# Kernel tuning notes

Hardware: AMD Instinct MI355X
Metric: run time of the kernel (lower is better)

Reference implementation:

```python
import jax, jax.numpy as jnp
import numpy as np

N = 50000        # num_nodes
D = 512          # input_dim == output_dim (residual update requires equality)
EU = 100000      # undirected edges; directed E = 2*EU = 200000
STEP = 0.5       # step_size


def setup_inputs() -> dict:
    key = jax.random.key(0)
    ks = jax.random.split(key, 5)
    x = jax.random.normal(ks[0], (N, D), jnp.float32)
    # symmetric edge list without self loops: store (s,d) then (d,s)
    src = jax.random.randint(ks[1], (EU,), 0, N, dtype=jnp.int32)
    off = jax.random.randint(ks[2], (EU,), 1, N, dtype=jnp.int32)
    dst = (src + off) % N
    edge_index = jnp.stack([jnp.concatenate([src, dst]),
                            jnp.concatenate([dst, src])])  # [2, 2*EU]
    # reverse-edge index: edge e < EU reverses to e+EU and vice versa
    ar = jnp.arange(EU, dtype=jnp.int32)
    right_idx = jnp.concatenate([ar + EU, ar])
    # params: nn.Linear(D, D) and sheaf_learner nn.Linear(2D, 1, bias=False)
    W_lin = jax.random.normal(ks[3], (D, D), jnp.float32) / np.sqrt(D)
    b_lin = jnp.zeros((D,), jnp.float32)
    w_sheaf = jax.random.normal(ks[4], (2 * D,), jnp.float32) / np.sqrt(2 * D)
    return {"x": x, "W_lin": W_lin, "b_lin": b_lin, "w_sheaf": w_sheaf,
            "edge_index": edge_index, "right_idx": right_idx}


def reference(x, W_lin, b_lin, w_sheaf, edge_index, right_idx):
    row, col = edge_index[0], edge_index[1]
    d = x.shape[1]
    # sheaf_learner(cat([x_row, x_col])) == (x @ w[:d])[row] + (x @ w[d:])[col]
    s = x @ w_sheaf[:d]                      # [N]
    t = x @ w_sheaf[d:]                      # [N]
    maps = jnp.tanh(s[row] + t[col])         # [E] scalar restriction maps
    # off-diagonal Laplacian values: -F_e(row) * F_reverse(e)
    non_diag = -maps * maps[right_idx]       # [E]
    diag_maps = jax.ops.segment_sum(maps ** 2, row, num_segments=N)  # [N]
    d_inv = (diag_maps + 1.0) ** -0.5        # [N]
    norm_maps = d_inv[row] * non_diag * d_inv[col]                   # [E]
    diag = d_inv * diag_maps * d_inv                                 # [N]
    # y = linear(x); L @ y done as diag term + edge scatter
    y = x @ W_lin.T + b_lin                  # [N, D]
    Ly = diag[:, None] * y + jax.ops.segment_sum(
        norm_maps[:, None] * y[col], row, num_segments=N)
    return x - STEP * Ly
```

## Files before the change

kernel.cpp:

```cpp
#include <hip/hip_runtime.h>
#include <hip/hip_bf16.h>
#include <cstdint>
#include <cstddef>


#define DD 512
#define STEPSZ 0.5f
#define SLOTS 32

typedef __bf16 bf16;
typedef __bf16 bf16x8 __attribute__((ext_vector_type(8)));
typedef __bf16 bf16x4 __attribute__((ext_vector_type(4)));
typedef float f32x4 __attribute__((ext_vector_type(4)));

#define GLOAD16(g, l)                                                     \
  __builtin_amdgcn_global_load_lds(                                       \
      (const __attribute__((address_space(1))) void*)(g),                 \
      (__attribute__((address_space(3))) void*)(l), 16, 0, 0)

__global__ __launch_bounds__(256) void k_convert_w(
    const float* __restrict__ w, bf16* __restrict__ wbf, int n) {
  int i = (blockIdx.x * 256 + threadIdx.x) * 4;
  if (i >= n) return;
  float4 v = *(const float4*)(w + i);
  bf16x4 p;
  p[0] = (bf16)v.x; p[1] = (bf16)v.y; p[2] = (bf16)v.z; p[3] = (bf16)v.w;
  *(bf16x4*)(wbf + i) = p;
}

__global__ __launch_bounds__(256) void k_convert_st(
    const float* __restrict__ x, const float* __restrict__ wsheaf,
    bf16* __restrict__ xbf, float* __restrict__ s, float* __restrict__ t,
    int n) {
  int lane = threadIdx.x & 63;
  int row = (blockIdx.x << 2) + (threadIdx.x >> 6);
  if (row >= n) return;
  const float* xr = x + (size_t)row * DD + lane * 8;
  float4 a = *(const float4*)xr;
  float4 b = *(const float4*)(xr + 4);
  bf16x8 p;
  p[0] = (bf16)a.x; p[1] = (bf16)a.y; p[2] = (bf16)a.z; p[3] = (bf16)a.w;
  p[4] = (bf16)b.x; p[5] = (bf16)b.y; p[6] = (bf16)b.z; p[7] = (bf16)b.w;
  *(bf16x8*)(xbf + (size_t)row * DD + lane * 8) = p;
  const float* w1 = wsheaf + lane * 8;
  const float* w2 = wsheaf + DD + lane * 8;
  float4 wa = *(const float4*)w1, wb = *(const float4*)(w1 + 4);
  float4 wc = *(const float4*)w2, wd = *(const float4*)(w2 + 4);
  float sv = a.x * wa.x + a.y * wa.y + a.z * wa.z + a.w * wa.w +
             b.x * wb.x + b.y * wb.y + b.z * wb.z + b.w * wb.w;
  float tv = a.x * wc.x + a.y * wc.y + a.z * wc.z + a.w * wc.w +
             b.x * wd.x + b.y * wd.y + b.z * wd.z + b.w * wd.w;
  #pragma unroll
  for (int o = 32; o > 0; o >>= 1) {
    sv += __shfl_xor(sv, o);
    tv += __shfl_xor(tv, o);
  }
  if (lane == 0) { s[row] = sv; t[row] = tv; }
}

__global__ __launch_bounds__(256) void k_fill(
    const int* __restrict__ ei, const float* __restrict__ s,
    const float* __restrict__ t, float* __restrict__ dmaps,
    int* __restrict__ fill, int* __restrict__ ccol, float* __restrict__ cval,
    int E) {
  int e = blockIdx.x * 256 + threadIdx.x;
  if (e >= E) return;
  int r = ei[e], c = ei[E + e];
  float sr = s[r], tc = t[c], sc = s[c], tr = t[r];
  float me = tanhf(sr + tc);
  float mr = tanhf(sc + tr);
  atomicAdd(dmaps + r, me * me);
  int p = atomicAdd(fill + r, 1);
  if (p < SLOTS) {
    ccol[(size_t)r * SLOTS + p] = c;
    cval[(size_t)r * SLOTS + p] = -me * mr;
  }
}

__global__ __launch_bounds__(256) void k_gemm(
    const bf16* __restrict__ xbf, const bf16* __restrict__ wbf,
    const float* __restrict__ bias, bf16* __restrict__ y, int M, int nwg) {
  __shared__ bf16 lds[16384];
  int orig = blockIdx.x;
  int q = nwg >> 3, r = nwg & 7;
  int xcd = orig & 7;
  int wgid = (xcd < r ? xcd * (q + 1) : r * (q + 1) + (xcd - r) * q) +
             (orig >> 3);
  int bm = wgid >> 2, bn = wgid & 3;
  int tid = threadIdx.x, w = tid >> 6, lane = tid & 63;
  int wr = w >> 1, wc = w & 1;
  int l7 = lane & 7, lhi = lane >> 4;

  int srow = lane >> 3;
  int kc = l7 ^ srow;
  const bf16* gA[4];
  const bf16* gB[4];
  bf16* lA[4];
  bf16* lB[4];
  #pragma unroll
  for (int j = 0; j < 4; ++j) {
    int rloc = w * 32 + j * 8 + srow;
    int ga = bm * 128 + rloc;
    if (ga > M - 1) ga = M - 1;
    gA[j] = xbf + (size_t)ga * DD + kc * 8;
    gB[j] = wbf + (size_t)(bn * 128 + rloc) * DD + kc * 8;
    lA[j] = lds + (w * 32 + j * 8) * 64;
    lB[j] = lds + 8192 + (w * 32 + j * 8) * 64;
  }

  f32x4 acc[4][4] = {};
  int arow = (wr * 64 + (lane & 15)) * 64;
  int brow = (wc * 64 + (lane & 15)) * 64;

  for (int k0 = 0; k0 < DD; k0 += 64) {
    #pragma unroll
    for (int j = 0; j < 4; ++j) {
      GLOAD16(gA[j] + k0, lA[j]);
      GLOAD16(gB[j] + k0, lB[j]);
    }
    __syncthreads();
    #pragma unroll
    for (int kw = 0; kw < 2; ++kw) {
      int sl = ((kw * 4 + lhi) ^ l7) * 8;
      bf16x8 af[4], bfr[4];
      #pragma unroll
      for (int m = 0; m < 4; ++m)
        af[m] = *(const bf16x8*)(lds + arow + m * 16 * 64 + sl);
      #pragma unroll
      for (int nn = 0; nn < 4; ++nn)
        bfr[nn] = *(const bf16x8*)(lds + 8192 + brow + nn * 16 * 64 + sl);
      #pragma unroll
      for (int m = 0; m < 4; ++m)
        #pragma unroll
        for (int nn = 0; nn < 4; ++nn)
          acc[m][nn] = __builtin_amdgcn_mfma_f32_16x16x32_bf16(
              af[m], bfr[nn], acc[m][nn], 0, 0, 0);
    }
    __syncthreads();
  }

  float bv[4];
  #pragma unroll
  for (int nn = 0; nn < 4; ++nn)
    bv[nn] = bias[bn * 128 + wc * 64 + nn * 16 + (lane & 15)];
  bf16* reg = lds + w * 4096;
  #pragma unroll
  for (int m = 0; m < 4; ++m)
    #pragma unroll
    for (int nn = 0; nn < 4; ++nn)
      #pragma unroll
      for (int rr = 0; rr < 4; ++rr) {
        int row = m * 16 + lhi * 4 + rr;
        int col = nn * 16 + (lane & 15);
        reg[row * 64 + (((col >> 3) ^ (row & 7)) << 3) + (col & 7)] =
            (bf16)(acc[m][nn][rr] + bv[nn]);
      }
  #pragma unroll
  for (int p = 0; p < 8; ++p) {
    int row = p * 8 + (lane >> 3);
    int slot = l7 ^ (row & 7);
    bf16x8 v = *(const bf16x8*)(reg + row * 64 + slot * 8);
    int grow = bm * 128 + wr * 64 + row;
    if (grow < M)
      *(bf16x8*)(y + (size_t)grow * DD + bn * 128 + wc * 64 + l7 * 8) = v;
  }
}

__global__ __launch_bounds__(256) void k_final(
    const float* __restrict__ x, const bf16* __restrict__ xb,
    const bf16* __restrict__ y, const float* __restrict__ dmaps,
    const int* __restrict__ fill, const int* __restrict__ ccol,
    const float* __restrict__ cval, float* __restrict__ out, int n,
    int use_bf) {
  int lane = threadIdx.x & 63;
  int row = (blockIdx.x << 2) + (threadIdx.x >> 6);
  if (row >= n) return;
  int c0 = lane * 8;
  bf16x8 yv = *(const bf16x8*)(y + (size_t)row * DD + c0);
  float dm = dmaps[row];
  float inv_r = rsqrtf(dm + 1.0f);
  float dg = dm / (dm + 1.0f);
  float acc[8];
  #pragma unroll
  for (int j = 0; j < 8; ++j) acc[j] = dg * (float)yv[j];
  int cnt = fill[row];
  if (cnt > SLOTS) cnt = SLOTS;
  const int* cc = ccol + (size_t)row * SLOTS;
  const float* cv = cval + (size_t)row * SLOTS;
  unsigned nm1 = (unsigned)(n - 1);
  for (int i = 0; i < cnt; i += 4) {
    int4 c4 = *(const int4*)(cc + i);
    float4 v4 = *(const float4*)(cv + i);
    int rem = cnt - i;
    unsigned ca = min((unsigned)c4.x, nm1);
    unsigned cb = min((unsigned)c4.y, nm1);
    unsigned cg = min((unsigned)c4.z, nm1);
    unsigned cd = min((unsigned)c4.w, nm1);
    bf16x8 na = *(const bf16x8*)(y + (size_t)ca * DD + c0);
    bf16x8 nb = *(const bf16x8*)(y + (size_t)cb * DD + c0);
    bf16x8 ng = *(const bf16x8*)(y + (size_t)cg * DD + c0);
    bf16x8 nd = *(const bf16x8*)(y + (size_t)cd * DD + c0);
    float va = rem > 0 ? v4.x * inv_r * rsqrtf(dmaps[ca] + 1.0f) : 0.0f;
    float vb = rem > 1 ? v4.y * inv_r * rsqrtf(dmaps[cb] + 1.0f) : 0.0f;
    float vg = rem > 2 ? v4.z * inv_r * rsqrtf(dmaps[cg] + 1.0f) : 0.0f;
    float vd = rem > 3 ? v4.w * inv_r * rsqrtf(dmaps[cd] + 1.0f) : 0.0f;
    #pragma unroll
    for (int j = 0; j < 8; ++j)
      acc[j] += va * (float)na[j] + vb * (float)nb[j] + vg * (float)ng[j] +
                vd * (float)nd[j];
  }
  float xr[8];
  if (use_bf) {
    bf16x8 xv = *(const bf16x8*)(xb + (size_t)row * DD + c0);
    #pragma unroll
    for (int j = 0; j < 8; ++j) xr[j] = (float)xv[j];
  } else {
    const float* xp = x + (size_t)row * DD + c0;
    float4 xa = *(const float4*)xp, xbv = *(const float4*)(xp + 4);
    xr[0] = xa.x; xr[1] = xa.y; xr[2] = xa.z; xr[3] = xa.w;
    xr[4] = xbv.x; xr[5] = xbv.y; xr[6] = xbv.z; xr[7] = xbv.w;
  }
  float4 o1, o2;
  o1.x = xr[0] - STEPSZ * acc[0]; o1.y = xr[1] - STEPSZ * acc[1];
  o1.z = xr[2] - STEPSZ * acc[2]; o1.w = xr[3] - STEPSZ * acc[3];
  o2.x = xr[4] - STEPSZ * acc[4]; o2.y = xr[5] - STEPSZ * acc[5];
  o2.z = xr[6] - STEPSZ * acc[6]; o2.w = xr[7] - STEPSZ * acc[7];
  float* outr = out + (size_t)row * DD + c0;
  *(float4*)outr = o1;
  *(float4*)(outr + 4) = o2;
}

extern "C" void kernel_launch(void* const* d_in, const int* in_sizes, int n_in,
                              void* d_out, int out_size, void* d_ws,
                              size_t ws_size, hipStream_t stream) {
  const float* x = (const float*)d_in[0];
  const float* W = (const float*)d_in[1];
  const float* b = (const float*)d_in[2];
  const float* wsheaf = (const float*)d_in[3];
  const int* ei = (const int*)d_in[4];
  const int* right = (const int*)d_in[5];
  (void)right;
  int N = in_sizes[0] / DD;
  int E = in_sizes[5];

  char* ws = (char*)d_ws;
  size_t p = 0;
  auto alloc = [&](size_t bytes) -> char* {
    char* r = ws + p;
    p += (bytes + 255) & ~(size_t)255;
    return r;
  };
  bf16* yb = (bf16*)alloc((size_t)N * DD * 2);
  float* cval = (float*)alloc((size_t)N * SLOTS * 4);
  int* ccol = (int*)alloc((size_t)N * SLOTS * 4);
  float* s = (float*)alloc((size_t)N * 4);
  float* t = (float*)alloc((size_t)N * 4);
  bf16* wbf = (bf16*)alloc((size_t)DD * DD * 2);
  char* zblock = alloc((size_t)N * 8);
  float* diag_maps = (float*)zblock;
  int* fill = (int*)(zblock + (size_t)N * 4);

  size_t xbf_bytes = (size_t)N * DD * 2;
  int use_bf = (p + xbf_bytes) <= ws_size;
  bf16* xbf = use_bf ? (bf16*)alloc(xbf_bytes) : (bf16*)d_out;

  hipMemsetAsync(zblock, 0, (size_t)N * 8, stream);
  k_convert_w<<<(DD * DD / 4 + 255) / 256, 256, 0, stream>>>(W, wbf, DD * DD);
  k_convert_st<<<(N + 3) / 4, 256, 0, stream>>>(x, wsheaf, xbf, s, t, N);
  k_fill<<<(E + 255) / 256, 256, 0, stream>>>(ei, s, t, diag_maps, fill, ccol,
                                              cval, E);
  int MT = (N + 127) / 128;
  int nwg = MT * 4;
  k_gemm<<<nwg, 256, 0, stream>>>(xbf, wbf, b, yb, N, nwg);
  k_final<<<(N + 3) / 4, 256, 0, stream>>>(x, xbf, yb, diag_maps, fill, ccol,
                                           cval, (float*)d_out, N, use_bf);
}
```

Baseline: 168.9 us.

## Reassociate Laplacian and linear layer: gather on x, then GEMM with fused residual epilogue

Uses L(xWᵀ+b) = (Lx)Wᵀ + rowsum(L)·b. A new gather kernel aggregates the bf16 x over neighbours and writes a per-row coefficient sum. The GEMM then multiplies the aggregated rows by W and writes x − step·(result + cb·bias) straight to the fp32 output. This drops the separate final kernel and the y round trip, and it reads the residual x in full fp32. The cost is a scalar, strided fp32 epilogue that reads x and writes out inside the GEMM, plus an extra bf16 intermediate write and read.

After: 184.6 us. +9.3%, slower.

```diff
diff --git a/kernel.cpp b/kernel.cpp
--- a/kernel.cpp
+++ b/kernel.cpp
@@ -77,9 +77,61 @@
   }
 }
 
+__global__ __launch_bounds__(256) void k_gather(
+    const bf16* __restrict__ xb, const float* __restrict__ dmaps,
+    const int* __restrict__ fill, const int* __restrict__ ccol,
+    const float* __restrict__ cval, bf16* __restrict__ u,
+    float* __restrict__ cb, int n) {
+  int lane = threadIdx.x & 63;
+  int row = (blockIdx.x << 2) + (threadIdx.x >> 6);
+  if (row >= n) return;
+  int c0 = lane * 8;
+  float dm = dmaps[row];
+  float inv_r = rsqrtf(dm + 1.0f);
+  float dg = dm / (dm + 1.0f);
+  bf16x8 xv = *(const bf16x8*)(xb + (size_t)row * DD + c0);
+  float acc[8];
+  #pragma unroll
+  for (int j = 0; j < 8; ++j) acc[j] = dg * (float)xv[j];
+  int cnt = fill[row];
+  if (cnt > SLOTS) cnt = SLOTS;
+  const int* cc = ccol + (size_t)row * SLOTS;
+  const float* cv = cval + (size_t)row * SLOTS;
+  unsigned nm1 = (unsigned)(n - 1);
+  float cbs = 0.0f;
+  for (int i = 0; i < cnt; i += 4) {
+    int4 c4 = *(const int4*)(cc + i);
+    float4 v4 = *(const float4*)(cv + i);
+    int rem = cnt - i;
+    unsigned ca = min((unsigned)c4.x, nm1);
+    unsigned cbi = min((unsigned)c4.y, nm1);
+    unsigned cg = min((unsigned)c4.z, nm1);
+    unsigned cd = min((unsigned)c4.w, nm1);
+    bf16x8 na = *(const bf16x8*)(xb + (size_t)ca * DD + c0);
+    bf16x8 nb = *(const bf16x8*)(xb + (size_t)cbi * DD + c0);
+    bf16x8 ng = *(const bf16x8*)(xb + (size_t)cg * DD + c0);
+    bf16x8 nd = *(const bf16x8*)(xb + (size_t)cd * DD + c0);
+    float va = rem > 0 ? v4.x * inv_r * rsqrtf(dmaps[ca] + 1.0f) : 0.0f;
+    float vb = rem > 1 ? v4.y * inv_r * rsqrtf(dmaps[cbi] + 1.0f) : 0.0f;
+    float vg = rem > 2 ? v4.z * inv_r * rsqrtf(dmaps[cg] + 1.0f) : 0.0f;
+    float vd = rem > 3 ? v4.w * inv_r * rsqrtf(dmaps[cd] + 1.0f) : 0.0f;
+    cbs += va + vb + vg + vd;
+    #pragma unroll
+    for (int j = 0; j < 8; ++j)
+      acc[j] += va * (float)na[j] + vb * (float)nb[j] + vg * (float)ng[j] +
+                vd * (float)nd[j];
+  }
+  bf16x8 o;
+  #pragma unroll
+  for (int j = 0; j < 8; ++j) o[j] = (bf16)acc[j];
+  *(bf16x8*)(u + (size_t)row * DD + c0) = o;
+  if (lane == 0) cb[row] = dg + cbs;
+}
+
 __global__ __launch_bounds__(256) void k_gemm(
-    const bf16* __restrict__ xbf, const bf16* __restrict__ wbf,
-    const float* __restrict__ bias, bf16* __restrict__ y, int M, int nwg) {
+    const bf16* __restrict__ ub, const bf16* __restrict__ wbf,
+    const float* __restrict__ bias, const float* __restrict__ x,
+    const float* __restrict__ cb, float* __restrict__ out, int M, int nwg) {
   __shared__ bf16 lds[16384];
   int orig = blockIdx.x;
   int q = nwg >> 3, r = nwg & 7;
@@ -102,7 +154,7 @@
     int rloc = w * 32 + j * 8 + srow;
     int ga = bm * 128 + rloc;
     if (ga > M - 1) ga = M - 1;
-    gA[j] = xbf + (size_t)ga * DD + kc * 8;
+    gA[j] = ub + (size_t)ga * DD + kc * 8;
     gB[j] = wbf + (size_t)(bn * 128 + rloc) * DD + kc * 8;
     lA[j] = lds + (w * 32 + j * 8) * 64;
     lB[j] = lds + 8192 + (w * 32 + j * 8) * 64;
@@ -143,91 +195,25 @@
   #pragma unroll
   for (int nn = 0; nn < 4; ++nn)
     bv[nn] = bias[bn * 128 + wc * 64 + nn * 16 + (lane & 15)];
-  bf16* reg = lds + w * 4096;
-  #pragma unroll
-  for (int m = 0; m < 4; ++m)
-    #pragma unroll
-    for (int nn = 0; nn < 4; ++nn)
-      #pragma unroll
-      for (int rr = 0; rr < 4; ++rr) {
-        int row = m * 16 + lhi * 4 + rr;
-        int col = nn * 16 + (lane & 15);
-        reg[row * 64 + (((col >> 3) ^ (row & 7)) << 3) + (col & 7)] =
-            (bf16)(acc[m][nn][rr] + bv[nn]);
+  int gc0 = bn * 128 + wc * 64 + (lane & 15);
+  #pragma unroll
+  for (int m = 0; m < 4; ++m) {
+    #pragma unroll
+    for (int rr = 0; rr < 4; ++rr) {
+      int gr = bm * 128 + wr * 64 + m * 16 + lhi * 4 + rr;
+      if (gr < M) {
+        float cbv = cb[gr];
+        const float* xrow = x + (size_t)gr * DD;
+        float* orow = out + (size_t)gr * DD;
+        #pragma unroll
+        for (int nn = 0; nn < 4; ++nn) {
+          int gcol = gc0 + nn * 16;
+          orow[gcol] =
+              xrow[gcol] - STEPSZ * (acc[m][nn][rr] + cbv * bv[nn]);
+        }
       }
-  #pragma unroll
-  for (int p = 0; p < 8; ++p) {
-    int row = p * 8 + (lane >> 3);
-    int slot = l7 ^ (row & 7);
-    bf16x8 v = *(const bf16x8*)(reg + row * 64 + slot * 8);
-    int grow = bm * 128 + wr * 64 + row;
-    if (grow < M)
-      *(bf16x8*)(y + (size_t)grow * DD + bn * 128 + wc * 64 + l7 * 8) = v;
-  }
-}
-
-__global__ __launch_bounds__(256) void k_final(
-    const float* __restrict__ x, const bf16* __restrict__ xb,
-    const bf16* __restrict__ y, const float* __restrict__ dmaps,
-    const int* __restrict__ fill, const int* __restrict__ ccol,
-    const float* __restrict__ cval, float* __restrict__ out, int n,
-    int use_bf) {
-  int lane = threadIdx.x & 63;
-  int row = (blockIdx.x << 2) + (threadIdx.x >> 6);
-  if (row >= n) return;
-  int c0 = lane * 8;
-  bf16x8 yv = *(const bf16x8*)(y + (size_t)row * DD + c0);
-  float dm = dmaps[row];
-  float inv_r = rsqrtf(dm + 1.0f);
-  float dg = dm / (dm + 1.0f);
-  float acc[8];
-  #pragma unroll
-  for (int j = 0; j < 8; ++j) acc[j] = dg * (float)yv[j];
-  int cnt = fill[row];
-  if (cnt > SLOTS) cnt = SLOTS;
-  const int* cc = ccol + (size_t)row * SLOTS;
-  const float* cv = cval + (size_t)row * SLOTS;
-  unsigned nm1 = (unsigned)(n - 1);
-  for (int i = 0; i < cnt; i += 4) {
-    int4 c4 = *(const int4*)(cc + i);
-    float4 v4 = *(const float4*)(cv + i);
-    int rem = cnt - i;
-    unsigned ca = min((unsigned)c4.x, nm1);
-    unsigned cb = min((unsigned)c4.y, nm1);
-    unsigned cg = min((unsigned)c4.z, nm1);
-    unsigned cd = min((unsigned)c4.w, nm1);
-    bf16x8 na = *(const bf16x8*)(y + (size_t)ca * DD + c0);
-    bf16x8 nb = *(const bf16x8*)(y + (size_t)cb * DD + c0);
-    bf16x8 ng = *(const bf16x8*)(y + (size_t)cg * DD + c0);
-    bf16x8 nd = *(const bf16x8*)(y + (size_t)cd * DD + c0);
-    float va = rem > 0 ? v4.x * inv_r * rsqrtf(dmaps[ca] + 1.0f) : 0.0f;
-    float vb = rem > 1 ? v4.y * inv_r * rsqrtf(dmaps[cb] + 1.0f) : 0.0f;
-    float vg = rem > 2 ? v4.z * inv_r * rsqrtf(dmaps[cg] + 1.0f) : 0.0f;
-    float vd = rem > 3 ? v4.w * inv_r * rsqrtf(dmaps[cd] + 1.0f) : 0.0f;
-    #pragma unroll
-    for (int j = 0; j < 8; ++j)
-      acc[j] += va * (float)na[j] + vb * (float)nb[j] + vg * (float)ng[j] +
-                vd * (float)nd[j];
-  }
-  float xr[8];
-  if (use_bf) {
-    bf16x8 xv = *(const bf16x8*)(xb + (size_t)row * DD + c0);
-    #pragma unroll
-    for (int j = 0; j < 8; ++j) xr[j] = (float)xv[j];
-  } else {
-    const float* xp = x + (size_t)row * DD + c0;
-    float4 xa = *(const float4*)xp, xbv = *(const float4*)(xp + 4);
-    xr[0] = xa.x; xr[1] = xa.y; xr[2] = xa.z; xr[3] = xa.w;
-    xr[4] = xbv.x; xr[5] = xbv.y; xr[6] = xbv.z; xr[7] = xbv.w;
-  }
-  float4 o1, o2;
-  o1.x = xr[0] - STEPSZ * acc[0]; o1.y = xr[1] - STEPSZ * acc[1];
-  o1.z = xr[2] - STEPSZ * acc[2]; o1.w = xr[3] - STEPSZ * acc[3];
-  o2.x = xr[4] - STEPSZ * acc[4]; o2.y = xr[5] - STEPSZ * acc[5];
-  o2.z = xr[6] - STEPSZ * acc[6]; o2.w = xr[7] - STEPSZ * acc[7];
-  float* outr = out + (size_t)row * DD + c0;
-  *(float4*)outr = o1;
-  *(float4*)(outr + 4) = o2;
+    }
+  }
 }
 
 extern "C" void kernel_launch(void* const* d_in, const int* in_sizes, int n_in,
@@ -250,28 +236,29 @@
     p += (bytes + 255) & ~(size_t)255;
     return r;
   };
-  bf16* yb = (bf16*)alloc((size_t)N * DD * 2);
+  bf16* ub = (bf16*)alloc((size_t)N * DD * 2);
   float* cval = (float*)alloc((size_t)N * SLOTS * 4);
   int* ccol = (int*)alloc((size_t)N * SLOTS * 4);
   float* s = (float*)alloc((size_t)N * 4);
   float* t = (float*)alloc((size_t)N * 4);
+  float* cb = (float*)alloc((size_t)N * 4);
   bf16* wbf = (bf16*)alloc((size_t)DD * DD * 2);
   char* zblock = alloc((size_t)N * 8);
   float* diag_maps = (float*)zblock;
   int* fill = (int*)(zblock + (size_t)N * 4);
 
   size_t xbf_bytes = (size_t)N * DD * 2;
-  int use_bf = (p + xbf_bytes) <= ws_size;
-  bf16* xbf = use_bf ? (bf16*)alloc(xbf_bytes) : (bf16*)d_out;
+  int xb_in_ws = (p + xbf_bytes) <= ws_size;
+  bf16* xbf = xb_in_ws ? (bf16*)alloc(xbf_bytes) : (bf16*)d_out;
 
   hipMemsetAsync(zblock, 0, (size_t)N * 8, stream);
   k_convert_w<<<(DD * DD / 4 + 255) / 256, 256, 0, stream>>>(W, wbf, DD * DD);
   k_convert_st<<<(N + 3) / 4, 256, 0, stream>>>(x, wsheaf, xbf, s, t, N);
   k_fill<<<(E + 255) / 256, 256, 0, stream>>>(ei, s, t, diag_maps, fill, ccol,
                                               cval, E);
+  k_gather<<<(N + 3) / 4, 256, 0, stream>>>(xbf, diag_maps, fill, ccol, cval,
+                                            ub, cb, N);
   int MT = (N + 127) / 128;
   int nwg = MT * 4;
-  k_gemm<<<nwg, 256, 0, stream>>>(xbf, wbf, b, yb, N, nwg);
-  k_final<<<(N + 3) / 4, 256, 0, stream>>>(x, xbf, yb, diag_maps, fill, ccol,
-                                           cval, (float*)d_out, N, use_bf);
-}
+  k_gemm<<<nwg, 256, 0, stream>>>(ub, wbf, b, x, cb, (float*)d_out, N, nwg);
+}
```
